# Kernel optimization log

Hardware: AMD Instinct MI355X
Metric: run time of the kernel (lower is better)

The kernel has to match this reference:

```python
import jax, jax.numpy as jnp
import numpy as np

B, Z, H, T = 256, 512, 2048, 16
EPS = 1e-5

def _normalize(v):
    return v / (jnp.linalg.norm(v) + 1e-12)

def setup_inputs() -> dict:
    key = jax.random.key(0)
    ks = jax.random.split(key, 10)
    s = lambda fan: 1.0 / np.sqrt(fan)
    return {
        "z": jax.random.normal(ks[0], (B, Z), dtype=jnp.float32),
        "fc_w": jax.random.normal(ks[1], (Z, Z), dtype=jnp.float32) * s(Z),
        "fc_b": jnp.zeros((Z,), dtype=jnp.float32),
        "fc_u": _normalize(jax.random.normal(ks[2], (Z,), dtype=jnp.float32)),
        "w_ih": jax.random.normal(ks[3], (3 * H, Z), dtype=jnp.float32) * s(Z),
        "w_hh": jax.random.normal(ks[4], (3 * H, H), dtype=jnp.float32) * s(H),
        "b_ih": jnp.zeros((3 * H,), dtype=jnp.float32).at[H:2 * H].set(1.0),  # forget-gate bias init
        "b_hh": jnp.zeros((3 * H,), dtype=jnp.float32),
        "lin_w": jax.random.normal(ks[5], (Z, H), dtype=jnp.float32) * s(H),
        "lin_b": jnp.zeros((Z,), dtype=jnp.float32),
    }

def _spectral_norm(w, u):
    # one torch-style power iteration (u, v treated as constants)
    v = jax.lax.stop_gradient(_normalize(w.T @ u))
    u1 = jax.lax.stop_gradient(_normalize(w @ v))
    sigma = u1 @ (w @ v)
    return w / sigma

def reference(z, fc_w, fc_b, fc_u, w_ih, w_hh, b_ih, b_hh, lin_w, lin_b):
    # spectral-norm linear: h0 = z @ (W/sigma)^T + b
    w_sn = _spectral_norm(fc_w, fc_u)
    x0 = z @ w_sn.T + fc_b                      # [B, Z]
    h0 = jnp.zeros((B, H), dtype=z.dtype)       # initHidden

    def step(carry, _):
        x, h = carry
        gi = x @ w_ih.T + b_ih                  # [B, 3H]
        gh = h @ w_hh.T + b_hh                  # [B, 3H]
        i_r, i_z, i_n = jnp.split(gi, 3, axis=1)
        h_r, h_z, h_n = jnp.split(gh, 3, axis=1)
        r = jax.nn.sigmoid(i_r + h_r)
        u = jax.nn.sigmoid(i_z + h_z)
        n = jnp.tanh(i_n + r * h_n)
        h_new = (1.0 - u) * n + u * h
        x_new = h_new @ lin_w.T + lin_b         # [B, Z] fed back as next input
        return (x_new, h_new), x_new

    _, outs = jax.lax.scan(step, (x0, h0), None, length=T)  # [T, B, Z]

    # per-timestep BatchNorm1d(affine=False), training-mode batch stats
    mean = jnp.mean(outs, axis=1, keepdims=True)
    var = jnp.mean((outs - mean) ** 2, axis=1, keepdims=True)
    y = (outs - mean) / jnp.sqrt(var + EPS)     # [T, B, Z]

    y = jnp.transpose(y, (1, 0, 2))             # [B, T, Z]
    return y.reshape(-1, Z)                     # [B*T, Z]
```

## Files before the change

kernel.cpp:

```cpp
#include <hip/hip_runtime.h>
#include <hip/hip_bf16.h>
#include <cstdint>
#include <cstddef>

#define B_  256
#define Z_  512
#define H_  2048
#define T_  16
#define H3_ 6144

using short8  = __attribute__((ext_vector_type(8))) short;
using bf16x8  = __attribute__((ext_vector_type(8))) __bf16;
using f32x4   = __attribute__((ext_vector_type(4))) float;
using f32x16  = __attribute__((ext_vector_type(16))) float;

__device__ __forceinline__ f32x4 mfma_bf16(short8 a, short8 b, f32x4 c) {
  return __builtin_amdgcn_mfma_f32_16x16x32_bf16(
      __builtin_bit_cast(bf16x8, a), __builtin_bit_cast(bf16x8, b), c, 0, 0, 0);
}
__device__ __forceinline__ f32x16 mfma_bf16_32(short8 a, short8 b, f32x16 c) {
  return __builtin_amdgcn_mfma_f32_32x32x16_bf16(
      __builtin_bit_cast(bf16x8, a), __builtin_bit_cast(bf16x8, b), c, 0, 0, 0);
}

__device__ __forceinline__ unsigned short f2bf(float f) {
  unsigned int u = __builtin_bit_cast(unsigned int, f);
  u = (u + 0x7FFFu + ((u >> 16) & 1u)) >> 16;
  return (unsigned short)u;
}

__device__ __forceinline__ float sigmoidf_(float x) { return 1.0f / (1.0f + __expf(-x)); }

__device__ __forceinline__ int swz(int row, int chunk) {
  return row * 64 + ((chunk ^ (row & 7)) << 3);
}
__device__ __forceinline__ int swz128(int row, int chunk) {
  return row * 128 + ((chunk ^ (row & 7)) << 3);
}

__global__ __launch_bounds__(512, 1) void gru_step10(
    const unsigned short* __restrict__ A, int K,
    const unsigned short* __restrict__ Wr,
    const unsigned short* __restrict__ Wz,
    const unsigned short* __restrict__ Wn,
    const unsigned short* __restrict__ Whn,
    const float* __restrict__ cr, const float* __restrict__ cz,
    const float* __restrict__ cn, const float* __restrict__ chn,
    float hn_scale,
    const float* __restrict__ h_old,
    float* __restrict__ h_new,
    unsigned short* __restrict__ h_hist)
{
  __shared__ __align__(16) unsigned short sbuf[2][24576];
  float* red  = (float*)sbuf;
  float* LDSf = (float*)sbuf;
  const int bid = blockIdx.x, tid = threadIdx.x;
  const int xcd = bid & 7, rst = bid >> 3;
  const int m_idx = rst & 3, gg = rst >> 2;
  const int grp = gg * 8 + xcd;
  const int m0 = m_idx * 64;
  const int gh0 = grp * 32;
  const int wave = tid >> 6, lane = tid & 63;
  const int s4 = wave & 3, gp = wave >> 2;
  const int lh = lane >> 5, l31 = lane & 31;

  const int arow = tid >> 3, ac0 = (tid & 7) * 2;
  const int wrow = tid >> 2, wc0 = (tid & 3) * 4;
  const unsigned short* wsrc =
      (wave < 2) ? Wr : (wave < 4) ? Wz : (wave < 6) ? Wn : Whn;
  const size_t aoff = (size_t)(m0 + arow) * K;
  const size_t woff = (size_t)(gh0 + (wrow & 31)) * K;
  const int ad0 = swz128(arow, ac0), ad1 = swz128(arow, ac0 + 1);
  const int wd0 = 8192 + swz128(wrow, wc0 + 0);
  const int wd1 = 8192 + swz128(wrow, wc0 + 1);
  const int wd2 = 8192 + swz128(wrow, wc0 + 2);
  const int wd3 = 8192 + swz128(wrow, wc0 + 3);

  uint4 Ra0, Ra1, Rw0, Rw1, Rw2, Rw3;
#define LDSET(k0)                                              \
  {                                                            \
    const int kk_ = (k0);                                      \
    Ra0 = *(const uint4*)(A    + aoff + kk_ + (ac0    ) * 8);  \
    Ra1 = *(const uint4*)(A    + aoff + kk_ + (ac0 + 1) * 8);  \
    Rw0 = *(const uint4*)(wsrc + woff + kk_ + (wc0    ) * 8);  \
    Rw1 = *(const uint4*)(wsrc + woff + kk_ + (wc0 + 1) * 8);  \
    Rw2 = *(const uint4*)(wsrc + woff + kk_ + (wc0 + 2) * 8);  \
    Rw3 = *(const uint4*)(wsrc + woff + kk_ + (wc0 + 3) * 8);  \
  }
#define STAGE(b)                                               \
  {                                                            \
    unsigned short* p_ = sbuf[b];                              \
    *(uint4*)(p_ + ad0) = Ra0;                                 \
    *(uint4*)(p_ + ad1) = Ra1;                                 \
    *(uint4*)(p_ + wd0) = Rw0;                                 \
    *(uint4*)(p_ + wd1) = Rw1;                                 \
    *(uint4*)(p_ + wd2) = Rw2;                                 \
    *(uint4*)(p_ + wd3) = Rw3;                                 \
  }

  f32x16 a00 = {}, a01 = {}, a10 = {}, a11 = {};
  const int g0r = gp * 64, g1r = gp * 64 + 32;

#define COMP(b)                                                            \
  {                                                                        \
    const unsigned short* p_ = sbuf[b];                                    \
    _Pragma("unroll")                                                      \
    for (int ss = 0; ss < 2; ++ss) {                                       \
      const int ch = (s4 + ss * 4) * 2 + lh;                               \
      short8 af0 = *(const short8*)(p_ + swz128(l31, ch));                 \
      short8 af1 = *(const short8*)(p_ + swz128(32 + l31, ch));            \
      short8 wf0 = *(const short8*)(p_ + 8192 + swz128(g0r + l31, ch));    \
      short8 wf1 = *(const short8*)(p_ + 8192 + swz128(g1r + l31, ch));    \
      a00 = mfma_bf16_32(af0, wf0, a00);                                   \
      a01 = mfma_bf16_32(af0, wf1, a01);                                   \
      a10 = mfma_bf16_32(af1, wf0, a10);                                   \
      a11 = mfma_bf16_32(af1, wf1, a11);                                   \
    }                                                                      \
  }

  const int nIter = K >> 7;
  LDSET(0);
  for (int it = 0; it < nIter; ++it) {
    const int b = it & 1;
    STAGE(b);
    __syncthreads();
    if (it + 1 < nIter) LDSET((it + 1) << 7);
    COMP(b);
  }
#undef LDSET
#undef STAGE
#undef COMP

  __syncthreads();
  if (s4 != 0) {
    float* rp = red + ((s4 - 1) * 2 + gp) * 4096;
#pragma unroll
    for (int r = 0; r < 16; ++r) rp[(0 * 16 + r) * 64 + lane] = a00[r];
#pragma unroll
    for (int r = 0; r < 16; ++r) rp[(1 * 16 + r) * 64 + lane] = a01[r];
#pragma unroll
    for (int r = 0; r < 16; ++r) rp[(2 * 16 + r) * 64 + lane] = a10[r];
#pragma unroll
    for (int r = 0; r < 16; ++r) rp[(3 * 16 + r) * 64 + lane] = a11[r];
  }
  __syncthreads();
  if (s4 == 0) {
#pragma unroll
    for (int ss = 0; ss < 3; ++ss) {
      const float* rp = red + (ss * 2 + gp) * 4096;
#pragma unroll
      for (int r = 0; r < 16; ++r) a00[r] += rp[(0 * 16 + r) * 64 + lane];
#pragma unroll
      for (int r = 0; r < 16; ++r) a01[r] += rp[(1 * 16 + r) * 64 + lane];
#pragma unroll
      for (int r = 0; r < 16; ++r) a10[r] += rp[(2 * 16 + r) * 64 + lane];
#pragma unroll
      for (int r = 0; r < 16; ++r) a11[r] += rp[(3 * 16 + r) * 64 + lane];
    }
  }
  __syncthreads();
  if (s4 == 0) {
    const int gA2 = gp * 2, gB2 = gp * 2 + 1;
#pragma unroll
    for (int r = 0; r < 16; ++r) {
      const int trow = (r & 3) + 8 * (r >> 2) + 4 * lh;
      LDSf[(gA2 * 64 + trow     ) * 33 + l31] = a00[r];
      LDSf[(gB2 * 64 + trow     ) * 33 + l31] = a01[r];
      LDSf[(gA2 * 64 + 32 + trow) * 33 + l31] = a10[r];
      LDSf[(gB2 * 64 + 32 + trow) * 33 + l31] = a11[r];
    }
  }
  __syncthreads();
  {
    const int row = tid >> 3, c0 = (tid & 7) * 4;
    const int grow = m0 + row;
#pragma unroll
    for (int j = 0; j < 4; ++j) {
      const int col = c0 + j;
      const int gcol = gh0 + col;
      const float R   = sigmoidf_(LDSf[(0 * 64 + row) * 33 + col] + cr[gcol]);
      const float U   = sigmoidf_(LDSf[(1 * 64 + row) * 33 + col] + cz[gcol]);
      const float HNv = hn_scale * LDSf[(3 * 64 + row) * 33 + col] + chn[gcol];
      const float Nv  = tanhf(LDSf[(2 * 64 + row) * 33 + col] + cn[gcol] + R * HNv);
      const float ho  = h_old ? h_old[(size_t)grow * H_ + gcol] : 0.0f;
      const float hv  = (1.0f - U) * Nv + U * ho;
      h_new[(size_t)grow * H_ + gcol]  = hv;
      h_hist[(size_t)grow * H_ + gcol] = f2bf(hv);
    }
  }
}

__device__ __forceinline__ void dev_gemm64core(
    unsigned short* sA, unsigned short* sB,
    const unsigned short* __restrict__ A,
    const unsigned short* __restrict__ Bw,
    int K,
    const float* __restrict__ addsrc, int add_ld,
    const float* __restrict__ bias,
    unsigned short* __restrict__ out_bf,
    float* __restrict__ out_f, int ldo, int mi, int ni)
{
  const int tid  = threadIdx.x;
  const int m0   = mi * 64, n0 = ni * 64;
  const int wave = tid >> 6, lane = tid & 63;
  const int wr = wave & 1, wc = wave >> 1;
  const int q = lane >> 4, c16 = lane & 15;
  const int lr = tid >> 3, lc8 = tid & 7;
  f32x4 acc[2][2] = {};
  const size_t aoff = (size_t)(m0 + lr) * K;
  const size_t boff = (size_t)(n0 + lr) * K;
  const size_t s32  = (size_t)32 * K;

  uint4 ra0, ra1, rb0, rb1;
  auto LOAD = [&](int k0) {
    const int gc = k0 + lc8 * 8;
    ra0 = *(const uint4*)(A  + aoff + gc);
    ra1 = *(const uint4*)(A  + aoff + s32 + gc);
    rb0 = *(const uint4*)(Bw + boff + gc);
    rb1 = *(const uint4*)(Bw + boff + s32 + gc);
  };

  const int nIter = K >> 6;
  LOAD(0);
  for (int it = 0; it < nIter; ++it) {
    __syncthreads();
    *(uint4*)(sA + swz(lr, lc8))      = ra0;
    *(uint4*)(sA + swz(lr + 32, lc8)) = ra1;
    *(uint4*)(sB + swz(lr, lc8))      = rb0;
    *(uint4*)(sB + swz(lr + 32, lc8)) = rb1;
    __syncthreads();
    if (it + 1 < nIter) LOAD((it + 1) << 6);
#pragma unroll
    for (int kk = 0; kk < 2; ++kk) {
      short8 af0 = *(const short8*)(sA + swz(wr * 32 + c16,      kk * 4 + q));
      short8 af1 = *(const short8*)(sA + swz(wr * 32 + 16 + c16, kk * 4 + q));
      short8 bf0 = *(const short8*)(sB + swz(wc * 32 + c16,      kk * 4 + q));
      short8 bf1 = *(const short8*)(sB + swz(wc * 32 + 16 + c16, kk * 4 + q));
      acc[0][0] = mfma_bf16(af0, bf0, acc[0][0]);
      acc[0][1] = mfma_bf16(af0, bf1, acc[0][1]);
      acc[1][0] = mfma_bf16(af1, bf0, acc[1][0]);
      acc[1][1] = mfma_bf16(af1, bf1, acc[1][1]);
    }
  }
#pragma unroll
  for (int i = 0; i < 2; ++i) {
#pragma unroll
    for (int j = 0; j < 2; ++j) {
#pragma unroll
      for (int v = 0; v < 4; ++v) {
        const int row = m0 + wr * 32 + i * 16 + q * 4 + v;
        const int col = n0 + wc * 32 + j * 16 + c16;
        float val = acc[i][j][v];
        if (addsrc) val += addsrc[(size_t)row * add_ld + col];
        if (bias)   val += bias[col];
        if (out_f)  out_f[(size_t)row * ldo + col] = val;
        if (out_bf) out_bf[(size_t)row * ldo + col] = f2bf(val);
      }
    }
  }
}

__global__ __launch_bounds__(256) void gemm_wsum(
    const unsigned short* __restrict__ w_ih_q,
    const unsigned short* __restrict__ lin_wT_q,
    const float* __restrict__ w_hh,
    unsigned short* __restrict__ Wsum_r,
    unsigned short* __restrict__ Wsum_z,
    unsigned short* __restrict__ Wn_c)
{
  __shared__ unsigned short sA[64 * 64];
  __shared__ unsigned short sB[64 * 64];
  const int g = blockIdx.y >> 5, ni = blockIdx.y & 31;
  const float* adds = (g < 2) ? (w_hh + (size_t)g * H_ * H_) : nullptr;
  unsigned short* outw = (g == 0) ? Wsum_r : (g == 1) ? Wsum_z : Wn_c;
  dev_gemm64core(sA, sB, w_ih_q + (size_t)g * H_ * Z_, lin_wT_q, Z_,
                 adds, H_, nullptr, outw, nullptr, H_, blockIdx.x, ni);
}

__global__ __launch_bounds__(256) void gemm_bt64(
    const unsigned short* __restrict__ A,
    const unsigned short* __restrict__ Bw,
    int K,
    const float* __restrict__ bias,
    float* __restrict__ out_f, int ldo)
{
  __shared__ unsigned short sA[64 * 64];
  __shared__ unsigned short sB[64 * 64];
  dev_gemm64core(sA, sB, A, Bw, K, nullptr, 0, bias, nullptr, out_f, ldo,
                 blockIdx.x, blockIdx.y);
}

__global__ __launch_bounds__(256) void x0_sig(
    const unsigned short* __restrict__ A,
    const unsigned short* __restrict__ Bw,
    const float* __restrict__ t2,
    const float* __restrict__ bias,
    unsigned short* __restrict__ out_bf)
{
  __shared__ unsigned short sA[32 * 64];
  __shared__ unsigned short sB[64 * 64];
  __shared__ float red2[256];
  const int tid  = threadIdx.x;
  const int K = Z_;
  {
    float v0 = t2[tid], v1 = t2[tid + 256];
    red2[tid] = v0 * v0 + v1 * v1;
    __syncthreads();
    for (int s = 128; s > 0; s >>= 1) {
      if (tid < s) red2[tid] += red2[tid + s];
      __syncthreads();
    }
  }
  const float s2 = red2[0];
  const float scale = (sqrtf(s2) + 1e-12f) / s2;
  const int m0   = blockIdx.x * 32, n0 = blockIdx.y * 64;
  const int wave = tid >> 6, lane = tid & 63;
  const int wr = wave & 1, wc = wave >> 1;
  const int q = lane >> 4, c16 = lane & 15;
  const int lr = tid >> 3, lc8 = tid & 7;
  f32x4 acc0 = {}, acc1 = {};
  const size_t rowA  = (size_t)(m0 + lr) * K;
  const size_t rowB0 = (size_t)(n0 + lr) * K;
  const size_t rowB1 = (size_t)(n0 + 32 + lr) * K;
  for (int k0 = 0; k0 < K; k0 += 64) {
    const int gc = k0 + lc8 * 8;
    uint4 ra  = *(const uint4*)(A  + rowA  + gc);
    uint4 rb0 = *(const uint4*)(Bw + rowB0 + gc);
    uint4 rb1 = *(const uint4*)(Bw + rowB1 + gc);
    __syncthreads();
    *(uint4*)(sA + swz(lr, lc8))      = ra;
    *(uint4*)(sB + swz(lr, lc8))      = rb0;
    *(uint4*)(sB + swz(32 + lr, lc8)) = rb1;
    __syncthreads();
#pragma unroll
    for (int kk = 0; kk < 2; ++kk) {
      const int arow = wr * 16 + c16;
      short8 af = *(const short8*)(sA + swz(arow, kk * 4 + q));
      const int brow = wc * 32 + c16;
      short8 b0 = *(const short8*)(sB + swz(brow, kk * 4 + q));
      acc0 = mfma_bf16(af, b0, acc0);
      short8 b1 = *(const short8*)(sB + swz(brow + 16, kk * 4 + q));
      acc1 = mfma_bf16(af, b1, acc1);
    }
  }
#pragma unroll
  for (int cf = 0; cf < 2; ++cf) {
    f32x4 a = cf ? acc1 : acc0;
#pragma unroll
    for (int v = 0; v < 4; ++v) {
      const int row = m0 + wr * 16 + q * 4 + v;
      const int col = n0 + wc * 32 + cf * 16 + c16;
      out_bf[(size_t)row * Z_ + col] = f2bf(a[v] * scale + bias[col]);
    }
  }
}

__global__ __launch_bounds__(256) void prep_all(
    const float* __restrict__ z, const float* __restrict__ fc_w,
    const float* __restrict__ fc_u,
    const float* __restrict__ w_ih, const float* __restrict__ w_hh,
    const float* __restrict__ lin_w, const float* __restrict__ lin_b,
    const float* __restrict__ b_ih, const float* __restrict__ b_hh,
    unsigned short* __restrict__ z_q, unsigned short* __restrict__ fc_w_q,
    unsigned short* __restrict__ w_ih_q, unsigned short* __restrict__ w_hhn_q,
    unsigned short* __restrict__ lin_w_q, unsigned short* __restrict__ lin_wT_q,
    float* __restrict__ t1v,
    float* __restrict__ c0r, float* __restrict__ c0z, float* __restrict__ c0n,
    float* __restrict__ c1r, float* __restrict__ c1z, float* __restrict__ c1n,
    float* __restrict__ chn)
{
  __shared__ float sh[32 * 33];
  const int b = blockIdx.x, tid = threadIdx.x;
  if (b < 8576) {
    const int i = b * 256 + tid;
    const float4* src; ushort4* dst; int idx;
    if (i < 32768)        { src = (const float4*)z;     dst = (ushort4*)z_q;     idx = i; }
    else if (i < 98304)   { src = (const float4*)fc_w;  dst = (ushort4*)fc_w_q;  idx = i - 32768; }
    else if (i < 884736)  { src = (const float4*)w_ih;  dst = (ushort4*)w_ih_q;  idx = i - 98304; }
    else if (i < 1933312) { src = (const float4*)(w_hh + (size_t)2 * H_ * H_);
                            dst = (ushort4*)w_hhn_q;    idx = i - 884736; }
    else                  { src = (const float4*)lin_w; dst = (ushort4*)lin_w_q; idx = i - 1933312; }
    float4 v = src[idx];
    ushort4 o; o.x = f2bf(v.x); o.y = f2bf(v.y); o.z = f2bf(v.z); o.w = f2bf(v.w);
    dst[idx] = o;
  } else if (b < 9600) {
    const int tt = b - 8576;
    const int bx = tt >> 4, by = tt & 15;
    const int k0 = bx * 32, z0 = by * 32;
    const int tx = tid & 31, ty = tid >> 5;
#pragma unroll
    for (int j = 0; j < 4; ++j)
      sh[(ty + j * 8) * 33 + tx] = lin_w[(size_t)(z0 + ty + j * 8) * H_ + k0 + tx];
    __syncthreads();
#pragma unroll
    for (int j = 0; j < 4; ++j)
      lin_wT_q[(size_t)(k0 + ty + j * 8) * Z_ + z0 + tx] = f2bf(sh[tx * 33 + ty + j * 8]);
  } else if (b < 9608) {
    const int bb = b - 9600;
    const int lane = tid & 63, wv = tid >> 6;
    const int col = bb * 64 + lane;
    float s = 0.f;
    for (int r = wv * 128; r < wv * 128 + 128; ++r)
      s += fc_w[(size_t)r * Z_ + col] * fc_u[r];
    sh[wv * 64 + lane] = s;
    __syncthreads();
    if (wv == 0)
      t1v[col] = sh[lane] + sh[64 + lane] + sh[128 + lane] + sh[192 + lane];
  } else {
    const int bb = b - 9608;
    const int wave = tid >> 6, lane = tid & 63;
#pragma unroll
    for (int i = 0; i < 4; ++i) {
      int row = bb * 16 + wave * 4 + i;
      float s = 0.f;
      for (int c = lane; c < Z_; c += 64) s += w_ih[(size_t)row * Z_ + c] * lin_b[c];
#pragma unroll
      for (int off = 32; off > 0; off >>= 1) s += __shfl_down(s, off);
      if (lane == 0) {
        const int g = row >> 11, j = row & 2047;
        const float bi = b_ih[row], bh = b_hh[row];
        if (g == 0)      { c0r[j] = bi + bh; c1r[j] = bi + bh + s; }
        else if (g == 1) { c0z[j] = bi + bh; c1z[j] = bi + bh + s; }
        else             { c0n[j] = bi;      c1n[j] = bi + s;      chn[j] = bh; }
      }
    }
  }
}

__global__ void sigma2(const float* __restrict__ W, const float* __restrict__ t1,
                       float* __restrict__ t2) {
  __shared__ float red[256];
  const int tid = threadIdx.x;
  float p = 0.f;
  for (int c = tid; c < Z_; c += 256) { float v = t1[c]; p += v * v; }
  red[tid] = p;
  __syncthreads();
  for (int s = 128; s > 0; s >>= 1) {
    if (tid < s) red[tid] += red[tid + s];
    __syncthreads();
  }
  const float invn = 1.0f / (sqrtf(red[0]) + 1e-12f);
  const int lane = tid & 63, wv = tid >> 6;
  const int row = blockIdx.x * 4 + wv;
  float s = 0.f;
  for (int c = lane; c < Z_; c += 64) s += W[(size_t)row * Z_ + c] * t1[c];
#pragma unroll
  for (int off = 32; off > 0; off >>= 1) s += __shfl_down(s, off);
  if (lane == 0) t2[row] = s * invn;
}

__global__ __launch_bounds__(256) void bn_k(const float* __restrict__ outs,
                                            float* __restrict__ y) {
  __shared__ float s_sum[4][64], s_sq[4][64], s_mean[64], s_inv[64];
  const int t = blockIdx.x, zb = blockIdx.y;
  const int zl = threadIdx.x & 63, bp = threadIdx.x >> 6;
  const int z = zb * 64 + zl;
  float sum = 0.f, sq = 0.f;
  for (int b = bp * 64; b < bp * 64 + 64; ++b) {
    float v = outs[(size_t)(t * 256 + b) * Z_ + z];
    sum += v; sq += v * v;
  }
  s_sum[bp][zl] = sum; s_sq[bp][zl] = sq;
  __syncthreads();
  if (bp == 0) {
    float S = s_sum[0][zl] + s_sum[1][zl] + s_sum[2][zl] + s_sum[3][zl];
    float Q = s_sq[0][zl] + s_sq[1][zl] + s_sq[2][zl] + s_sq[3][zl];
    float mean = S * (1.0f / 256.0f);
    float var  = Q * (1.0f / 256.0f) - mean * mean;
    s_mean[zl] = mean;
    s_inv[zl]  = rsqrtf(var + 1e-5f);
  }
  __syncthreads();
  const float mean = s_mean[zl], inv = s_inv[zl];
  for (int b = bp * 64; b < bp * 64 + 64; ++b) {
    float v = outs[(size_t)(t * 256 + b) * Z_ + z];
    y[(size_t)(b * T_ + t) * Z_ + z] = (v - mean) * inv;
  }
}

extern "C" void kernel_launch(void* const* d_in, const int* in_sizes, int n_in,
                              void* d_out, int out_size, void* d_ws, size_t ws_size,
                              hipStream_t stream) {
  const float* z     = (const float*)d_in[0];
  const float* fc_w  = (const float*)d_in[1];
  const float* fc_b  = (const float*)d_in[2];
  const float* fc_u  = (const float*)d_in[3];
  const float* w_ih  = (const float*)d_in[4];
  const float* w_hh  = (const float*)d_in[5];
  const float* b_ih  = (const float*)d_in[6];
  const float* b_hh  = (const float*)d_in[7];
  const float* lin_w = (const float*)d_in[8];
  const float* lin_b = (const float*)d_in[9];
  float* out = (float*)d_out;

  char* ws = (char*)d_ws;
  size_t off = 0;
  auto alloc = [&](size_t bytes) -> void* {
    off = (off + 255) & ~(size_t)255;
    void* p = ws + off;
    off += bytes;
    return p;
  };
  unsigned short* w_ih_q   = (unsigned short*)alloc((size_t)H3_ * Z_ * 2);
  unsigned short* w_hhn_q  = (unsigned short*)alloc((size_t)H_ * H_ * 2);
  unsigned short* lin_w_q  = (unsigned short*)alloc((size_t)Z_ * H_ * 2);
  unsigned short* lin_wT_q = (unsigned short*)alloc((size_t)Z_ * H_ * 2);
  unsigned short* fc_w_q   = (unsigned short*)alloc((size_t)Z_ * Z_ * 2);
  unsigned short* z_q      = (unsigned short*)alloc((size_t)B_ * Z_ * 2);
  unsigned short* x0_q     = (unsigned short*)alloc((size_t)B_ * Z_ * 2);
  unsigned short* Wsum_r   = (unsigned short*)alloc((size_t)H_ * H_ * 2);
  unsigned short* Wsum_z   = (unsigned short*)alloc((size_t)H_ * H_ * 2);
  unsigned short* Wn_c     = (unsigned short*)alloc((size_t)H_ * H_ * 2);
  unsigned short* Hhist    = (unsigned short*)alloc((size_t)T_ * B_ * H_ * 2);
  float* h_f32 = (float*)alloc((size_t)2 * B_ * H_ * 4);
  float* outs  = (float*)alloc((size_t)T_ * B_ * Z_ * 4);
  float* c0r = (float*)alloc(H_ * 4);
  float* c0z = (float*)alloc(H_ * 4);
  float* c0n = (float*)alloc(H_ * 4);
  float* c1r = (float*)alloc(H_ * 4);
  float* c1z = (float*)alloc(H_ * 4);
  float* c1n = (float*)alloc(H_ * 4);
  float* chn = (float*)alloc(H_ * 4);
  float* t1v = (float*)alloc(Z_ * 4);
  float* t2v = (float*)alloc(Z_ * 4);
  (void)in_sizes; (void)n_in; (void)out_size; (void)ws_size;

  prep_all<<<9992, 256, 0, stream>>>(
      z, fc_w, fc_u, w_ih, w_hh, lin_w, lin_b, b_ih, b_hh,
      z_q, fc_w_q, w_ih_q, w_hhn_q, lin_w_q, lin_wT_q,
      t1v, c0r, c0z, c0n, c1r, c1z, c1n, chn);
  sigma2<<<128, 256, 0, stream>>>(fc_w, t1v, t2v);
  x0_sig<<<dim3(8, 8), 256, 0, stream>>>(z_q, fc_w_q, t2v, fc_b, x0_q);

  gemm_wsum<<<dim3(H_ / 64, 96), 256, 0, stream>>>(
      w_ih_q, lin_wT_q, w_hh, Wsum_r, Wsum_z, Wn_c);

  for (int t = 0; t < T_; ++t) {
    if (t == 0) {
      gru_step10<<<256, 512, 0, stream>>>(
          x0_q, Z_,
          w_ih_q, w_ih_q + (size_t)H_ * Z_, w_ih_q + (size_t)2 * H_ * Z_,
          w_ih_q ,
          c0r, c0z, c0n, chn, 0.0f, nullptr, h_f32, Hhist);
    } else {
      gru_step10<<<256, 512, 0, stream>>>(
          Hhist + (size_t)(t - 1) * B_ * H_, H_,
          Wsum_r, Wsum_z, Wn_c, w_hhn_q,
          c1r, c1z, c1n, chn, 1.0f,
          h_f32 + (size_t)((t - 1) & 1) * B_ * H_,
          h_f32 + (size_t)(t & 1) * B_ * H_,
          Hhist + (size_t)t * B_ * H_);
    }
  }

  gemm_bt64<<<dim3(T_ * B_ / 64, Z_ / 64), 256, 0, stream>>>(
      Hhist, lin_w_q, H_, lin_b, outs, Z_);

  bn_k<<<dim3(T_, Z_ / 64), 256, 0, stream>>>(outs, out);
}
```

Measured before the change: 477.8 us.

## Double GRU step block to 1024 threads with 8-way K split

The GRU step kernel now runs 16 waves per block instead of 8, so each wave takes one K-chunk of the 128-wide tile rather than two, and each thread loads fewer global elements per stage. The cross-wave reduction becomes an 8-way split done one accumulator at a time through LDS, with a barrier pair per accumulator. The epilogue is remapped so 1024 threads each handle 2 columns. The aim is more latency hiding and shorter per-wave MFMA chains, at the cost of more barriers and a larger reduction. The launch bound of 1024 threads with a minimum of 4 blocks also adds register pressure.

New measurement: 570.3 us. +19.4%, slower.

```diff
diff --git a/kernel.cpp b/kernel.cpp
--- a/kernel.cpp
+++ b/kernel.cpp
@@ -38,7 +38,7 @@
   return row * 128 + ((chunk ^ (row & 7)) << 3);
 }
 
-__global__ __launch_bounds__(512, 1) void gru_step10(
+__global__ __launch_bounds__(1024, 4) void gru_step11(
     const unsigned short* __restrict__ A, int K,
     const unsigned short* __restrict__ Wr,
     const unsigned short* __restrict__ Wz,
@@ -61,41 +61,33 @@
   const int m0 = m_idx * 64;
   const int gh0 = grp * 32;
   const int wave = tid >> 6, lane = tid & 63;
-  const int s4 = wave & 3, gp = wave >> 2;
+  const int sid = wave & 7, gp = wave >> 3;
   const int lh = lane >> 5, l31 = lane & 31;
 
-  const int arow = tid >> 3, ac0 = (tid & 7) * 2;
-  const int wrow = tid >> 2, wc0 = (tid & 3) * 4;
+  const int arow = tid >> 4, ac = tid & 15;
+  const int wrow = tid >> 3, wc0 = (tid & 7) * 2;
   const unsigned short* wsrc =
-      (wave < 2) ? Wr : (wave < 4) ? Wz : (wave < 6) ? Wn : Whn;
+      (wrow < 32) ? Wr : (wrow < 64) ? Wz : (wrow < 96) ? Wn : Whn;
   const size_t aoff = (size_t)(m0 + arow) * K;
   const size_t woff = (size_t)(gh0 + (wrow & 31)) * K;
-  const int ad0 = swz128(arow, ac0), ad1 = swz128(arow, ac0 + 1);
+  const int ad0 = swz128(arow, ac);
   const int wd0 = 8192 + swz128(wrow, wc0 + 0);
   const int wd1 = 8192 + swz128(wrow, wc0 + 1);
-  const int wd2 = 8192 + swz128(wrow, wc0 + 2);
-  const int wd3 = 8192 + swz128(wrow, wc0 + 3);
-
-  uint4 Ra0, Ra1, Rw0, Rw1, Rw2, Rw3;
+
+  uint4 Ra0, Rw0, Rw1;
 #define LDSET(k0)                                              \
   {                                                            \
     const int kk_ = (k0);                                      \
-    Ra0 = *(const uint4*)(A    + aoff + kk_ + (ac0    ) * 8);  \
-    Ra1 = *(const uint4*)(A    + aoff + kk_ + (ac0 + 1) * 8);  \
+    Ra0 = *(const uint4*)(A    + aoff + kk_ + ac * 8);         \
     Rw0 = *(const uint4*)(wsrc + woff + kk_ + (wc0    ) * 8);  \
     Rw1 = *(const uint4*)(wsrc + woff + kk_ + (wc0 + 1) * 8);  \
-    Rw2 = *(const uint4*)(wsrc + woff + kk_ + (wc0 + 2) * 8);  \
-    Rw3 = *(const uint4*)(wsrc + woff + kk_ + (wc0 + 3) * 8);  \
   }
 #define STAGE(b)                                               \
   {                                                            \
     unsigned short* p_ = sbuf[b];                              \
     *(uint4*)(p_ + ad0) = Ra0;                                 \
-    *(uint4*)(p_ + ad1) = Ra1;                                 \
     *(uint4*)(p_ + wd0) = Rw0;                                 \
     *(uint4*)(p_ + wd1) = Rw1;                                 \
-    *(uint4*)(p_ + wd2) = Rw2;                                 \
-    *(uint4*)(p_ + wd3) = Rw3;                                 \
   }
 
   f32x16 a00 = {}, a01 = {}, a10 = {}, a11 = {};
@@ -104,18 +96,15 @@
 #define COMP(b)                                                            \
   {                                                                        \
     const unsigned short* p_ = sbuf[b];                                    \
-    _Pragma("unroll")                                                      \
-    for (int ss = 0; ss < 2; ++ss) {                                       \
-      const int ch = (s4 + ss * 4) * 2 + lh;                               \
-      short8 af0 = *(const short8*)(p_ + swz128(l31, ch));                 \
-      short8 af1 = *(const short8*)(p_ + swz128(32 + l31, ch));            \
-      short8 wf0 = *(const short8*)(p_ + 8192 + swz128(g0r + l31, ch));    \
-      short8 wf1 = *(const short8*)(p_ + 8192 + swz128(g1r + l31, ch));    \
-      a00 = mfma_bf16_32(af0, wf0, a00);                                   \
-      a01 = mfma_bf16_32(af0, wf1, a01);                                   \
-      a10 = mfma_bf16_32(af1, wf0, a10);                                   \
-      a11 = mfma_bf16_32(af1, wf1, a11);                                   \
-    }                                                                      \
+    const int ch = sid * 2 + lh;                                           \
+    short8 af0 = *(const short8*)(p_ + swz128(l31, ch));                   \
+    short8 af1 = *(const short8*)(p_ + swz128(32 + l31, ch));              \
+    short8 wf0 = *(const short8*)(p_ + 8192 + swz128(g0r + l31, ch));      \
+    short8 wf1 = *(const short8*)(p_ + 8192 + swz128(g1r + l31, ch));      \
+    a00 = mfma_bf16_32(af0, wf0, a00);                                     \
+    a01 = mfma_bf16_32(af0, wf1, a01);                                     \
+    a10 = mfma_bf16_32(af1, wf0, a10);                                     \
+    a11 = mfma_bf16_32(af1, wf1, a11);                                     \
   }
 
   const int nIter = K >> 7;
@@ -132,34 +121,31 @@
 #undef COMP
 
   __syncthreads();
-  if (s4 != 0) {
-    float* rp = red + ((s4 - 1) * 2 + gp) * 4096;
-#pragma unroll
-    for (int r = 0; r < 16; ++r) rp[(0 * 16 + r) * 64 + lane] = a00[r];
-#pragma unroll
-    for (int r = 0; r < 16; ++r) rp[(1 * 16 + r) * 64 + lane] = a01[r];
-#pragma unroll
-    for (int r = 0; r < 16; ++r) rp[(2 * 16 + r) * 64 + lane] = a10[r];
-#pragma unroll
-    for (int r = 0; r < 16; ++r) rp[(3 * 16 + r) * 64 + lane] = a11[r];
-  }
-  __syncthreads();
-  if (s4 == 0) {
-#pragma unroll
-    for (int ss = 0; ss < 3; ++ss) {
-      const float* rp = red + (ss * 2 + gp) * 4096;
-#pragma unroll
-      for (int r = 0; r < 16; ++r) a00[r] += rp[(0 * 16 + r) * 64 + lane];
-#pragma unroll
-      for (int r = 0; r < 16; ++r) a01[r] += rp[(1 * 16 + r) * 64 + lane];
-#pragma unroll
-      for (int r = 0; r < 16; ++r) a10[r] += rp[(2 * 16 + r) * 64 + lane];
-#pragma unroll
-      for (int r = 0; r < 16; ++r) a11[r] += rp[(3 * 16 + r) * 64 + lane];
-    }
-  }
-  __syncthreads();
-  if (s4 == 0) {
+#define RED(accv)                                                          \
+  {                                                                        \
+    if (sid != 0) {                                                        \
+      float* rp = red + ((sid - 1) * 2 + gp) * 1024;                       \
+      _Pragma("unroll")                                                    \
+      for (int r = 0; r < 16; ++r) rp[r * 64 + lane] = accv[r];            \
+    }                                                                      \
+    __syncthreads();                                                       \
+    if (sid == 0) {                                                        \
+      _Pragma("unroll")                                                    \
+      for (int ss = 0; ss < 7; ++ss) {                                     \
+        const float* rp = red + (ss * 2 + gp) * 1024;                      \
+        _Pragma("unroll")                                                  \
+        for (int r = 0; r < 16; ++r) accv[r] += rp[r * 64 + lane];         \
+      }                                                                    \
+    }                                                                      \
+    __syncthreads();                                                       \
+  }
+  RED(a00)
+  RED(a01)
+  RED(a10)
+  RED(a11)
+#undef RED
+
+  if (sid == 0) {
     const int gA2 = gp * 2, gB2 = gp * 2 + 1;
 #pragma unroll
     for (int r = 0; r < 16; ++r) {
@@ -172,10 +158,10 @@
   }
   __syncthreads();
   {
-    const int row = tid >> 3, c0 = (tid & 7) * 4;
+    const int row = tid >> 4, c0 = (tid & 15) * 2;
     const int grow = m0 + row;
 #pragma unroll
-    for (int j = 0; j < 4; ++j) {
+    for (int j = 0; j < 2; ++j) {
       const int col = c0 + j;
       const int gcol = gh0 + col;
       const float R   = sigmoidf_(LDSf[(0 * 64 + row) * 33 + col] + cr[gcol]);
@@ -537,13 +523,13 @@
 
   for (int t = 0; t < T_; ++t) {
     if (t == 0) {
-      gru_step10<<<256, 512, 0, stream>>>(
+      gru_step11<<<256, 1024, 0, stream>>>(
           x0_q, Z_,
           w_ih_q, w_ih_q + (size_t)H_ * Z_, w_ih_q + (size_t)2 * H_ * Z_,
           w_ih_q ,
           c0r, c0z, c0n, chn, 0.0f, nullptr, h_f32, Hhist);
     } else {
-      gru_step10<<<256, 512, 0, stream>>>(
+      gru_step11<<<256, 1024, 0, stream>>>(
           Hhist + (size_t)(t - 1) * B_ * H_, H_,
           Wsum_r, Wsum_z, Wn_c, w_hhn_q,
           c1r, c1z, c1n, chn, 1.0f,
```
